# Performance work log

Measured on AMD Instinct MI355X. Metric: run time of the kernel, lower is better.

## Reference

```python
import jax, jax.numpy as jnp
import numpy as np

VOCAB, EMB, HID, T, B = 50257, 512, 1024, 512, 64
R, ALPHA = 8, 16
SCALE = ALPHA / R  # LoRA scaling


def _layer_params(key, in_dim, hid):
    ks = jax.random.split(key, 8)
    stdv = 1.0 / np.sqrt(hid)
    u = lambda k, s: jax.random.uniform(k, s, jnp.float32, -stdv, stdv)
    return dict(
        W_ih=u(ks[0], (4 * hid, in_dim)), b_ih=u(ks[1], (4 * hid,)),
        A_ih=jax.random.normal(ks[2], (R, in_dim)) * 0.01,
        B_ih=jax.random.normal(ks[3], (4 * hid, R)) * 0.01,
        W_hh=u(ks[4], (4 * hid, hid)), b_hh=u(ks[5], (4 * hid,)),
        A_hh=jax.random.normal(ks[6], (R, hid)) * 0.01,
        B_hh=jax.random.normal(ks[7], (4 * hid, R)) * 0.01,
    )


def setup_inputs() -> dict:
    key = jax.random.key(0)
    k_emb, kx, kl, k0, k1 = jax.random.split(key, 5)
    emb = jax.random.normal(k_emb, (VOCAB, EMB), jnp.float32)
    emb = emb.at[0].set(0.0)  # padding_idx=0
    x = jax.random.randint(kx, (B, T), 0, VOCAB)
    lengths = jax.random.randint(kl, (B,), 1, T + 1)
    p0 = _layer_params(k0, EMB, HID)
    p1 = _layer_params(k1, HID, HID)
    inp = {"x": x, "lengths": lengths, "emb": emb}
    for name, p in (("0", p0), ("1", p1)):
        for k, v in p.items():
            inp[f"{k}{name}"] = v
    return inp


def _run_layer(seq, W_ih, b_ih, A_ih, B_ih, W_hh, b_hh, A_hh, B_hh):
    # seq: [T, B, D] -> [T, B, H]; LoRA linear: x@W^T + b + (x@A^T)@B^T * scale
    x_proj = (jnp.einsum('tbd,gd->tbg', seq, W_ih) + b_ih
              + jnp.einsum('tbr,gr->tbg', jnp.einsum('tbd,rd->tbr', seq, A_ih), B_ih) * SCALE)

    def step(carry, xp):
        h, c = carry
        gates = (xp + h @ W_hh.T + b_hh + ((h @ A_hh.T) @ B_hh.T) * SCALE)
        i, f, g, o = jnp.split(gates, 4, axis=-1)
        c = jax.nn.sigmoid(f) * c + jax.nn.sigmoid(i) * jnp.tanh(g)
        h = jax.nn.sigmoid(o) * jnp.tanh(c)
        return (h, c), h

    nb = seq.shape[1]
    hid = W_hh.shape[1]
    h0 = jnp.zeros((nb, hid), seq.dtype)
    _, hs = jax.lax.scan(step, (h0, h0), x_proj)
    return hs


def reference(x, lengths, emb,
              W_ih0, b_ih0, A_ih0, B_ih0, W_hh0, b_hh0, A_hh0, B_hh0,
              W_ih1, b_ih1, A_ih1, B_ih1, W_hh1, b_hh1, A_hh1, B_hh1):
    # embedding lookup (dropout in eval mode = identity)
    h_in = emb[x]                       # [B, T, E]
    h_in = jnp.swapaxes(h_in, 0, 1)     # [T, B, E] for scan
    h_in = _run_layer(h_in, W_ih0, b_ih0, A_ih0, B_ih0, W_hh0, b_hh0, A_hh0, B_hh0)
    h_in = _run_layer(h_in, W_ih1, b_ih1, A_ih1, B_ih1, W_hh1, b_hh1, A_hh1, B_hh1)
    idx = jnp.clip(lengths - 1, 0, None)            # [B]
    last_h = h_in[idx, jnp.arange(h_in.shape[1])]   # [B, H]
    return last_h
```

## Files before the change

### kernel.cpp

```cpp
#include <hip/hip_runtime.h>
#include <stdint.h>

typedef _Float16 f16;
typedef _Float16 f16x8 __attribute__((ext_vector_type(8)));
typedef float f32x4 __attribute__((ext_vector_type(4)));

#define NBATCH 64

__device__ __forceinline__ float sigmoidf_(float x) {
    return 1.0f / (1.0f + __expf(-x));
}
__device__ __forceinline__ float tanh_(float x) {
    x = fminf(fmaxf(x, -15.0f), 15.0f);
    float e = __expf(2.0f * x);
    return (e - 1.0f) / (e + 1.0f);
}

__global__ __launch_bounds__(256) void fold_lora(
    const float* __restrict__ W, const float* __restrict__ Bm,
    const float* __restrict__ Am, f16* __restrict__ dst, int K) {
    int cid = blockIdx.x * 256 + threadIdx.x;
    int kc = K >> 3;
    int r = cid / kc;
    int k0 = (cid - r * kc) * 8;
    float bb[8];
#pragma unroll
    for (int j = 0; j < 8; j++) bb[j] = Bm[r * 8 + j];
#pragma unroll
    for (int i = 0; i < 8; i++) {
        float s = 0.0f;
#pragma unroll
        for (int j = 0; j < 8; j++) s += bb[j] * Am[j * K + k0 + i];
        float v = W[(size_t)r * K + k0 + i] + 2.0f * s;
        dst[(size_t)r * K + k0 + i] = (f16)v;
    }
}

__global__ __launch_bounds__(256) void init_misc(
    const float* __restrict__ bih0, const float* __restrict__ bhh0,
    const float* __restrict__ bih1, const float* __restrict__ bhh1,
    float* __restrict__ bsum0, float* __restrict__ bsum1,
    int* __restrict__ flags0, int* __restrict__ flags1,
    float* __restrict__ c0, float* __restrict__ c1) {
    int i = blockIdx.x * 256 + threadIdx.x;
    if (i < 4096) {
        bsum0[i] = bih0[i] + bhh0[i];
        bsum1[i] = bih1[i] + bhh1[i];
    }
    if (i < 256) { flags0[i] = 0; flags1[i] = 0; }
    c0[i] = 0.0f;
    c1[i] = 0.0f;
}

__global__ __launch_bounds__(256) void embed_gather(
    const int* __restrict__ x, const float* __restrict__ emb,
    f16* __restrict__ seqc, int t0) {
    int lt = blockIdx.x;
    int t = t0 + lt;
#pragma unroll
    for (int c = 0; c < 16; c++) {
        int lin = c * 256 + threadIdx.x;
        int b = lin >> 6;
        int e0 = (lin & 63) * 8;
        int tok = x[b * 512 + t];
        const float* src = emb + (size_t)tok * 512 + e0;
        f16x8 v;
#pragma unroll
        for (int i = 0; i < 8; i++) v[i] = (f16)src[i];
        *(f16x8*)&seqc[((size_t)lt * 64 + b) * 512 + e0] = v;
    }
}

__global__ __launch_bounds__(256) void gemm_nt(
    const f16* __restrict__ A, const f16* __restrict__ Bw,
    float* __restrict__ C, int K, int mtmask, int mtshift) {
    __shared__ f16 As[128 * 40];
    __shared__ f16 Bs[128 * 40];
    int bid = blockIdx.x;
    int mt = bid & mtmask, nt = bid >> mtshift;
    int tid = threadIdx.x;
    int w = tid >> 6, lane = tid & 63;
    int lm = lane & 15, lq = lane >> 4;
    int wm = (w >> 1) * 64, wn = (w & 1) * 64;
    f32x4 acc[4][4];
#pragma unroll
    for (int i = 0; i < 4; i++)
#pragma unroll
        for (int j = 0; j < 4; j++) acc[i][j] = f32x4{0.f, 0.f, 0.f, 0.f};
    const f16* Ab = A + (size_t)mt * 128 * K;
    const f16* Bb = Bw + (size_t)nt * 128 * K;
    int nkc = K >> 5;
    for (int kc = 0; kc < nkc; kc++) {
#pragma unroll
        for (int i = 0; i < 2; i++) {
            int cid = tid + i * 256;
            int r = cid >> 2, c8 = (cid & 3) * 8;
            *(f16x8*)&As[r * 40 + c8] = *(const f16x8*)&Ab[(size_t)r * K + kc * 32 + c8];
            *(f16x8*)&Bs[r * 40 + c8] = *(const f16x8*)&Bb[(size_t)r * K + kc * 32 + c8];
        }
        __syncthreads();
        f16x8 af[4], bf[4];
#pragma unroll
        for (int mi = 0; mi < 4; mi++)
            af[mi] = *(const f16x8*)&As[(wm + mi * 16 + lm) * 40 + lq * 8];
#pragma unroll
        for (int ni = 0; ni < 4; ni++)
            bf[ni] = *(const f16x8*)&Bs[(wn + ni * 16 + lm) * 40 + lq * 8];
#pragma unroll
        for (int mi = 0; mi < 4; mi++)
#pragma unroll
            for (int ni = 0; ni < 4; ni++)
                acc[mi][ni] = __builtin_amdgcn_mfma_f32_16x16x32_f16(
                    af[mi], bf[ni], acc[mi][ni], 0, 0, 0);
        __syncthreads();
    }
#pragma unroll
    for (int mi = 0; mi < 4; mi++)
#pragma unroll
        for (int ni = 0; ni < 4; ni++)
#pragma unroll
            for (int r = 0; r < 4; r++) {
                int m = mt * 128 + wm + mi * 16 + lq * 4 + r;
                int n = nt * 128 + wn + ni * 16 + lm;
                int gate = n >> 10, u = n & 1023;
                C[(size_t)m * 4096 + u * 4 + gate] = acc[mi][ni][r];
            }
}


__device__ __forceinline__ void stage_h(f16* hbuf, const uint32_t* hx, int slot,
                                        int bg, int tid) {
    const uint64_t* hp = (const uint64_t*)hx + (size_t)slot * (NBATCH * 256);
#pragma unroll
    for (int i = 0; i < 16; i++) {
        int lin = tid + i * 256;
        int b = lin >> 8, d = lin & 255;
        uint64_t v = __hip_atomic_load(hp + (size_t)(bg * 16 + b) * 256 + d,
                                       __ATOMIC_RELAXED, __HIP_MEMORY_SCOPE_AGENT);
        *(uint64_t*)((char*)hbuf + (size_t)b * 2064 + (size_t)d * 8) = v;
    }
}

__device__ __forceinline__ f32x4 recur_mfma(const f16* hb, const f16x8* wf) {
    f32x4 a0 = f32x4{0.f, 0.f, 0.f, 0.f};
    f32x4 a1 = f32x4{0.f, 0.f, 0.f, 0.f};
    f32x4 a2 = f32x4{0.f, 0.f, 0.f, 0.f};
    f32x4 a3 = f32x4{0.f, 0.f, 0.f, 0.f};
#pragma unroll
    for (int kk = 0; kk < 32; kk += 4) {
        a0 = __builtin_amdgcn_mfma_f32_16x16x32_f16(*(const f16x8*)(hb + (kk + 0) * 32), wf[kk + 0], a0, 0, 0, 0);
        a1 = __builtin_amdgcn_mfma_f32_16x16x32_f16(*(const f16x8*)(hb + (kk + 1) * 32), wf[kk + 1], a1, 0, 0, 0);
        a2 = __builtin_amdgcn_mfma_f32_16x16x32_f16(*(const f16x8*)(hb + (kk + 2) * 32), wf[kk + 2], a2, 0, 0, 0);
        a3 = __builtin_amdgcn_mfma_f32_16x16x32_f16(*(const f16x8*)(hb + (kk + 3) * 32), wf[kk + 3], a3, 0, 0, 0);
    }
    return (a0 + a1) + (a2 + a3);
}

__device__ __forceinline__ void chain_loop(
    const float* __restrict__ xp, const f16* __restrict__ Wh,
    const float* __restrict__ bsum, uint32_t* __restrict__ hexch,
    int* __restrict__ flags, float* __restrict__ cstate,
    int t0, int smask, const int* __restrict__ lengths,
    float* __restrict__ dout, int bid, int nsteps,
    f16* hbuf, float* xch) {
    int tid = threadIdx.x;
    int g = tid >> 6, lane = tid & 63;
    int lm = lane & 15, lq = lane >> 4;
    int bg = bid >> 6, jg = bid & 63;

    f16x8 wfrag[32];
    {
        int grow = g * 1024 + jg * 16 + lm;
        const f16* wp = Wh + (size_t)grow * 1024 + lq * 8;
#pragma unroll
        for (int kk = 0; kk < 32; kk++) wfrag[kk] = *(const f16x8*)(wp + kk * 32);
    }
    int eb = tid >> 4, eu = tid & 15;
    int batch = bg * 16 + eb;
    int hidx = jg * 16 + eu;
    float bias[4];
#pragma unroll
    for (int g2 = 0; g2 < 4; g2++) bias[g2] = bsum[g2 * 1024 + hidx];
    int mylen = (lengths != nullptr) ? lengths[batch] : -1;
    float c = (t0 > 0) ? cstate[(size_t)batch * 1024 + hidx] : 0.0f;
    const int myflag = bg * 64 + jg;

    for (int lt = 0; lt < nsteps; lt++) {
        int t = t0 + lt;
        const f32x4 xpv = *(const f32x4*)(xp + ((size_t)lt * 64 + batch) * 4096 + (hidx << 2));
        f32x4 pre = f32x4{0.f, 0.f, 0.f, 0.f};
        if (t > 0) {
            if (tid < 64) {
                const int* fl = flags + bg * 64;
                for (;;) {
                    int v = __hip_atomic_load(fl + tid, __ATOMIC_RELAXED,
                                              __HIP_MEMORY_SCOPE_AGENT);
                    if (__all(v >= t)) break;
                    __builtin_amdgcn_s_sleep(1);
                }
            }
            __syncthreads();
            stage_h(hbuf, hexch, (t - 1) & smask, bg, tid);
            __syncthreads();
            pre = recur_mfma(&hbuf[lm * 1032 + lq * 8], wfrag);
        }
#pragma unroll
        for (int r = 0; r < 4; r++)
            xch[(g * 16 + lq * 4 + r) * 16 + lm] = pre[r];
        __syncthreads();
        float pg[4];
#pragma unroll
        for (int g2 = 0; g2 < 4; g2++)
            pg[g2] = xch[(g2 * 16 + eb) * 16 + eu] + xpv[g2] + bias[g2];
        float iv = sigmoidf_(pg[0]);
        float fv = sigmoidf_(pg[1]);
        float gv = tanh_(pg[2]);
        float ov = sigmoidf_(pg[3]);
        c = fv * c + iv * gv;
        float h = ov * tanh_(c);
        float hn = __shfl_xor(h, 1);
        if ((tid & 1) == 0) {
            uint16_t lo, hi;
            {
                f16 a = (f16)h, b2 = (f16)hn;
                lo = *(uint16_t*)&a; hi = *(uint16_t*)&b2;
            }
            uint32_t pk = (uint32_t)lo | ((uint32_t)hi << 16);
            __hip_atomic_store(
                hexch + (size_t)(t & smask) * (NBATCH * 512)
                      + (size_t)batch * 512 + (hidx >> 1),
                pk, __ATOMIC_RELAXED, __HIP_MEMORY_SCOPE_AGENT);
        }
        if (dout != nullptr && t == mylen - 1)
            dout[(size_t)batch * 1024 + hidx] = h;
        __syncthreads();
        if (tid == 0)
            __hip_atomic_store(flags + myflag, t + 1, __ATOMIC_RELAXED,
                               __HIP_MEMORY_SCOPE_AGENT);
    }
    cstate[(size_t)batch * 1024 + hidx] = c;
}

__global__ __launch_bounds__(256, 2) void lstm_dual(
    const float* __restrict__ xpA, const f16* __restrict__ WhA,
    const float* __restrict__ bsA, uint32_t* __restrict__ hxA,
    int* __restrict__ flagsA, float* __restrict__ cstA, int t0a, int smaskA,
    const float* __restrict__ xpB, const f16* __restrict__ WhB,
    const float* __restrict__ bsB, uint32_t* __restrict__ hxB,
    int* __restrict__ flagsB, float* __restrict__ cstB, int t0b,
    const int* __restrict__ lengths, float* __restrict__ dout, int nsteps) {
    __shared__ f16 hbuf[16 * 1032];
    __shared__ float xch[4 * 16 * 16];
    const int cid = blockIdx.x;
    if (cid < 256) {
        if (t0a < 0) return;
        chain_loop(xpA, WhA, bsA, hxA, flagsA, cstA, t0a, smaskA,
                   nullptr, nullptr, cid, nsteps, hbuf, xch);
    } else {
        if (t0b < 0) return;
        chain_loop(xpB, WhB, bsB, hxB, flagsB, cstB, t0b, 1,
                   lengths, dout, cid - 256, nsteps, hbuf, xch);
    }
}

extern "C" void kernel_launch(void* const* d_in, const int* in_sizes, int n_in,
                              void* d_out, int out_size, void* d_ws, size_t ws_size,
                              hipStream_t stream) {
    const int*   x     = (const int*)d_in[0];
    const int*   len   = (const int*)d_in[1];
    const float* emb   = (const float*)d_in[2];
    const float* W_ih0 = (const float*)d_in[3];
    const float* b_ih0 = (const float*)d_in[4];
    const float* A_ih0 = (const float*)d_in[5];
    const float* B_ih0 = (const float*)d_in[6];
    const float* W_hh0 = (const float*)d_in[7];
    const float* b_hh0 = (const float*)d_in[8];
    const float* A_hh0 = (const float*)d_in[9];
    const float* B_hh0 = (const float*)d_in[10];
    const float* W_ih1 = (const float*)d_in[11];
    const float* b_ih1 = (const float*)d_in[12];
    const float* A_ih1 = (const float*)d_in[13];
    const float* B_ih1 = (const float*)d_in[14];
    const float* W_hh1 = (const float*)d_in[15];
    const float* b_hh1 = (const float*)d_in[16];
    const float* A_hh1 = (const float*)d_in[17];
    const float* B_hh1 = (const float*)d_in[18];

    char* ws = (char*)d_ws;
    size_t off = 0;
    auto alloc = [&](size_t bytes) {
        size_t o = off;
        off += (bytes + 255) & ~(size_t)255;
        return o;
    };
    f16*   W0f    = (f16*)(ws + alloc((size_t)4096 * 512 * 2));
    f16*   Wh0f   = (f16*)(ws + alloc((size_t)4096 * 1024 * 2));
    f16*   W1f    = (f16*)(ws + alloc((size_t)4096 * 1024 * 2));
    f16*   Wh1f   = (f16*)(ws + alloc((size_t)4096 * 1024 * 2));
    float* bsum0  = (float*)(ws + alloc(4096 * 4));
    float* bsum1  = (float*)(ws + alloc(4096 * 4));
    int*   flags0 = (int*)(ws + alloc(4096));
    int*   flags1 = (int*)(ws + alloc(4096));
    float* c0st   = (float*)(ws + alloc((size_t)64 * 1024 * 4));
    float* c1st   = (float*)(ws + alloc((size_t)64 * 1024 * 4));
    f16*   hx1    = (f16*)(ws + alloc((size_t)2 * 64 * 1024 * 2));

    int CHv = 64;
    {
        auto al = [](size_t b) { return (b + 255) & ~(size_t)255; };
        size_t need = off
            + al((size_t)64 * 64 * 512 * 2)
            + al((size_t)64 * 64 * 1024 * 2)
            + 2 * al((size_t)64 * 64 * 4096 * 4);
        if (ws_size < need) CHv = 32;
    }
    const int NCHv = 512 / CHv;
    f16*   seqc = (f16*)(ws + alloc((size_t)CHv * 64 * 512 * 2));
    f16*   h0c  = (f16*)(ws + alloc((size_t)CHv * 64 * 1024 * 2));
    float* xp0c = (float*)(ws + alloc((size_t)CHv * 64 * 4096 * 4));
    float* xp1c = (float*)(ws + alloc((size_t)CHv * 64 * 4096 * 4));
    const int mtiles  = (CHv * 64) / 128;
    const int mtmask  = mtiles - 1;
    const int mtshift = (CHv == 64) ? 5 : 4;
    (void)in_sizes; (void)n_in; (void)out_size;

    fold_lora<<<1024, 256, 0, stream>>>(W_ih0, B_ih0, A_ih0, W0f, 512);
    fold_lora<<<2048, 256, 0, stream>>>(W_hh0, B_hh0, A_hh0, Wh0f, 1024);
    fold_lora<<<2048, 256, 0, stream>>>(W_ih1, B_ih1, A_ih1, W1f, 1024);
    fold_lora<<<2048, 256, 0, stream>>>(W_hh1, B_hh1, A_hh1, Wh1f, 1024);
    init_misc<<<256, 256, 0, stream>>>(b_ih0, b_hh0, b_ih1, b_hh1,
                                       bsum0, bsum1, flags0, flags1, c0st, c1st);

    for (int c = 0; c <= NCHv; c++) {
        if (c < NCHv) {
            embed_gather<<<CHv, 256, 0, stream>>>(x, emb, seqc, c * CHv);
            gemm_nt<<<mtiles * 32, 256, 0, stream>>>(seqc, W0f, xp0c, 512,
                                                     mtmask, mtshift);
        }
        if (c > 0)
            gemm_nt<<<mtiles * 32, 256, 0, stream>>>(h0c, W1f, xp1c, 1024,
                                                     mtmask, mtshift);
        lstm_dual<<<512, 256, 0, stream>>>(
            xp0c, Wh0f, bsum0, (uint32_t*)h0c, flags0, c0st,
            (c < NCHv) ? c * CHv : -1, CHv - 1,
            xp1c, Wh1f, bsum1, (uint32_t*)hx1, flags1, c1st,
            (c > 0) ? (c - 1) * CHv : -1,
            len, (float*)d_out, CHv);
    }
}
```

Before: 6.009 ms.

## Overlap input-projection GEMMs with LSTM recurrence inside the persistent kernel

Adds 256 extra blocks to the lstm_dual launch. These blocks compute the next chunk's layer-0 input projection and the current chunk's layer-1 input projection while the recurrent chains run. Layer-1 tiles spin on the layer-0 step flags and read the hidden states with atomic loads, so they can start before the chunk finishes. The xp and seqc buffers are now double-buffered to make this possible. The change costs extra workspace, needs three blocks resident per CU, and adds spin-wait contention beside the latency-critical recurrent chains.

```diff
diff --git a/kernel.cpp b/kernel.cpp
--- a/kernel.cpp
+++ b/kernel.cpp
@@ -71,13 +71,11 @@
     }
 }
 
-__global__ __launch_bounds__(256) void gemm_nt(
-    const f16* __restrict__ A, const f16* __restrict__ Bw,
-    float* __restrict__ C, int K, int mtmask, int mtshift) {
-    __shared__ f16 As[128 * 40];
-    __shared__ f16 Bs[128 * 40];
-    int bid = blockIdx.x;
-    int mt = bid & mtmask, nt = bid >> mtshift;
+template <bool ATOMIC_A>
+__device__ __forceinline__ void gemm_tile(
+    f16* As, f16* Bs, const f16* Aplain, const uint64_t* A64,
+    const f16* __restrict__ Bw, float* __restrict__ C,
+    int K, int mt, int nt) {
     int tid = threadIdx.x;
     int w = tid >> 6, lane = tid & 63;
     int lm = lane & 15, lq = lane >> 4;
@@ -87,7 +85,8 @@
     for (int i = 0; i < 4; i++)
 #pragma unroll
         for (int j = 0; j < 4; j++) acc[i][j] = f32x4{0.f, 0.f, 0.f, 0.f};
-    const f16* Ab = A + (size_t)mt * 128 * K;
+    const f16* Ab = Aplain + (size_t)mt * 128 * K;
+    const uint64_t* Ab64 = A64 + (size_t)mt * 128 * (K >> 2);
     const f16* Bb = Bw + (size_t)nt * 128 * K;
     int nkc = K >> 5;
     for (int kc = 0; kc < nkc; kc++) {
@@ -95,8 +94,20 @@
         for (int i = 0; i < 2; i++) {
             int cid = tid + i * 256;
             int r = cid >> 2, c8 = (cid & 3) * 8;
-            *(f16x8*)&As[r * 40 + c8] = *(const f16x8*)&Ab[(size_t)r * K + kc * 32 + c8];
-            *(f16x8*)&Bs[r * 40 + c8] = *(const f16x8*)&Bb[(size_t)r * K + kc * 32 + c8];
+            if (ATOMIC_A) {
+                size_t o = (size_t)r * (K >> 2) + (size_t)kc * 8 + (c8 >> 2);
+                uint64_t v0 = __hip_atomic_load(Ab64 + o, __ATOMIC_RELAXED,
+                                                __HIP_MEMORY_SCOPE_AGENT);
+                uint64_t v1 = __hip_atomic_load(Ab64 + o + 1, __ATOMIC_RELAXED,
+                                                __HIP_MEMORY_SCOPE_AGENT);
+                *(uint64_t*)&As[r * 40 + c8] = v0;
+                *(uint64_t*)&As[r * 40 + c8 + 4] = v1;
+            } else {
+                *(f16x8*)&As[r * 40 + c8] =
+                    *(const f16x8*)&Ab[(size_t)r * K + kc * 32 + c8];
+            }
+            *(f16x8*)&Bs[r * 40 + c8] =
+                *(const f16x8*)&Bb[(size_t)r * K + kc * 32 + c8];
         }
         __syncthreads();
         f16x8 af[4], bf[4];
@@ -125,6 +136,15 @@
                 int gate = n >> 10, u = n & 1023;
                 C[(size_t)m * 4096 + u * 4 + gate] = acc[mi][ni][r];
             }
+}
+
+__global__ __launch_bounds__(256) void gemm_nt(
+    const f16* __restrict__ A, const f16* __restrict__ Bw,
+    float* __restrict__ C, int K, int mtmask, int mtshift) {
+    __shared__ __align__(16) char smem[20480];
+    int bid = blockIdx.x;
+    gemm_tile<false>((f16*)smem, (f16*)(smem + 10240), A, nullptr, Bw, C, K,
+                     bid & mtmask, bid >> mtshift);
 }
 
 
@@ -241,25 +261,66 @@
     cstate[(size_t)batch * 1024 + hidx] = c;
 }
 
-__global__ __launch_bounds__(256, 2) void lstm_dual(
+__global__ __launch_bounds__(256, 3) void lstm_dual(
     const float* __restrict__ xpA, const f16* __restrict__ WhA,
     const float* __restrict__ bsA, uint32_t* __restrict__ hxA,
     int* __restrict__ flagsA, float* __restrict__ cstA, int t0a, int smaskA,
     const float* __restrict__ xpB, const f16* __restrict__ WhB,
     const float* __restrict__ bsB, uint32_t* __restrict__ hxB,
     int* __restrict__ flagsB, float* __restrict__ cstB, int t0b,
-    const int* __restrict__ lengths, float* __restrict__ dout, int nsteps) {
-    __shared__ f16 hbuf[16 * 1032];
-    __shared__ float xch[4 * 16 * 16];
+    const int* __restrict__ lengths, float* __restrict__ dout, int nsteps,
+    const f16* __restrict__ seqcN, const f16* __restrict__ W0f,
+    const f16* __restrict__ W1f, float* __restrict__ xp0out,
+    float* __restrict__ xp1out, int tpb, int mtmaskG, int mtshiftG) {
+    __shared__ __align__(16) char smem[37376];
     const int cid = blockIdx.x;
     if (cid < 256) {
         if (t0a < 0) return;
         chain_loop(xpA, WhA, bsA, hxA, flagsA, cstA, t0a, smaskA,
-                   nullptr, nullptr, cid, nsteps, hbuf, xch);
-    } else {
+                   nullptr, nullptr, cid, nsteps,
+                   (f16*)smem, (float*)(smem + 33024));
+    } else if (cid < 512) {
         if (t0b < 0) return;
         chain_loop(xpB, WhB, bsB, hxB, flagsB, cstB, t0b, 1,
-                   lengths, dout, cid - 256, nsteps, hbuf, xch);
+                   lengths, dout, cid - 256, nsteps,
+                   (f16*)smem, (float*)(smem + 33024));
+    } else {
+        f16* As = (f16*)smem;
+        f16* Bs = (f16*)(smem + 10240);
+        const int gb = cid - 512;
+        if (seqcN != nullptr) {
+            for (int j = 0; j < tpb; j++) {
+                int id = gb * tpb + j;
+                gemm_tile<false>(As, Bs, seqcN, nullptr, W0f, xp0out, 512,
+                                 id & mtmaskG, id >> mtshiftG);
+            }
+        }
+        if (t0a >= 0) {
+            for (int j = 0; j < tpb; j++) {
+                int id = gb * tpb + j;
+                int mt = id & mtmaskG, nt = id >> mtshiftG;
+                int tneed = t0a + 2 * mt + 2;
+                if (threadIdx.x < 64) {
+                    int tx = threadIdx.x;
+                    for (;;) {
+                        int v0 = __hip_atomic_load(flagsA + tx, __ATOMIC_RELAXED,
+                                                   __HIP_MEMORY_SCOPE_AGENT);
+                        int v1 = __hip_atomic_load(flagsA + 64 + tx, __ATOMIC_RELAXED,
+                                                   __HIP_MEMORY_SCOPE_AGENT);
+                        int v2 = __hip_atomic_load(flagsA + 128 + tx, __ATOMIC_RELAXED,
+                                                   __HIP_MEMORY_SCOPE_AGENT);
+                        int v3 = __hip_atomic_load(flagsA + 192 + tx, __ATOMIC_RELAXED,
+                                                   __HIP_MEMORY_SCOPE_AGENT);
+                        int mn = min(min(v0, v1), min(v2, v3));
+                        if (__all(mn >= tneed)) break;
+                        __builtin_amdgcn_s_sleep(2);
+                    }
+                }
+                __syncthreads();
+                gemm_tile<true>(As, Bs, nullptr, (const uint64_t*)hxA, W1f,
+                                xp1out, 1024, mt, nt);
+            }
+        }
     }
 }
 
@@ -305,23 +366,26 @@
     float* c1st   = (float*)(ws + alloc((size_t)64 * 1024 * 4));
     f16*   hx1    = (f16*)(ws + alloc((size_t)2 * 64 * 1024 * 2));
 
-    int CHv = 64;
-    {
-        auto al = [](size_t b) { return (b + 255) & ~(size_t)255; };
-        size_t need = off
-            + al((size_t)64 * 64 * 512 * 2)
-            + al((size_t)64 * 64 * 1024 * 2)
-            + 2 * al((size_t)64 * 64 * 4096 * 4);
-        if (ws_size < need) CHv = 32;
-    }
+    auto al = [](size_t b) { return (b + 255) & ~(size_t)255; };
+    auto need_for = [&](size_t CH) {
+        return off + 2 * al(CH * 64 * 512 * 2)
+                   + al(CH * 64 * 1024 * 2)
+                   + 4 * al(CH * 64 * 4096 * 4);
+    };
+    int CHv = (ws_size >= need_for(64)) ? 64 : 32;
     const int NCHv = 512 / CHv;
-    f16*   seqc = (f16*)(ws + alloc((size_t)CHv * 64 * 512 * 2));
+    const size_t seqcE = (size_t)CHv * 64 * 512;
+    const size_t xpE   = (size_t)CHv * 64 * 4096;
+    f16*   seqc = (f16*)(ws + alloc(2 * al(seqcE * 2)) );
     f16*   h0c  = (f16*)(ws + alloc((size_t)CHv * 64 * 1024 * 2));
-    float* xp0c = (float*)(ws + alloc((size_t)CHv * 64 * 4096 * 4));
-    float* xp1c = (float*)(ws + alloc((size_t)CHv * 64 * 4096 * 4));
+    float* xp0  = (float*)(ws + alloc(2 * al(xpE * 4)));
+    float* xp1  = (float*)(ws + alloc(2 * al(xpE * 4)));
+    const size_t seqcStride = al(seqcE * 2) / sizeof(f16);
+    const size_t xpStride   = al(xpE * 4) / sizeof(float);
     const int mtiles  = (CHv * 64) / 128;
     const int mtmask  = mtiles - 1;
     const int mtshift = (CHv == 64) ? 5 : 4;
+    const int tpb     = (mtiles * 32) / 256;
     (void)in_sizes; (void)n_in; (void)out_size;
 
     fold_lora<<<1024, 256, 0, stream>>>(W_ih0, B_ih0, A_ih0, W0f, 512);
@@ -331,20 +395,23 @@
     init_misc<<<256, 256, 0, stream>>>(b_ih0, b_hh0, b_ih1, b_hh1,
                                        bsum0, bsum1, flags0, flags1, c0st, c1st);
 
+    embed_gather<<<CHv, 256, 0, stream>>>(x, emb, seqc, 0);
+    gemm_nt<<<mtiles * 32, 256, 0, stream>>>(seqc, W0f, xp0, 512,
+                                             mtmask, mtshift);
     for (int c = 0; c <= NCHv; c++) {
-        if (c < NCHv) {
-            embed_gather<<<CHv, 256, 0, stream>>>(x, emb, seqc, c * CHv);
-            gemm_nt<<<mtiles * 32, 256, 0, stream>>>(seqc, W0f, xp0c, 512,
-                                                     mtmask, mtshift);
-        }
-        if (c > 0)
-            gemm_nt<<<mtiles * 32, 256, 0, stream>>>(h0c, W1f, xp1c, 1024,
-                                                     mtmask, mtshift);
-        lstm_dual<<<512, 256, 0, stream>>>(
-            xp0c, Wh0f, bsum0, (uint32_t*)h0c, flags0, c0st,
-            (c < NCHv) ? c * CHv : -1, CHv - 1,
-            xp1c, Wh1f, bsum1, (uint32_t*)hx1, flags1, c1st,
-            (c > 0) ? (c - 1) * CHv : -1,
-            len, (float*)d_out, CHv);
-    }
-}
+        if (c + 1 < NCHv)
+            embed_gather<<<CHv, 256, 0, stream>>>(
+                x, emb, seqc + ((c + 1) & 1) * seqcStride, (c + 1) * CHv);
+        const bool g0 = (c + 1) < NCHv;
+        lstm_dual<<<768, 256, 0, stream>>>(
+            xp0 + (c & 1) * xpStride, Wh0f, bsum0, (uint32_t*)h0c,
+            flags0, c0st, (c < NCHv) ? c * CHv : -1, CHv - 1,
+            xp1 + ((c + 1) & 1) * xpStride, Wh1f, bsum1, (uint32_t*)hx1,
+            flags1, c1st, (c > 0) ? (c - 1) * CHv : -1,
+            len, (float*)d_out, CHv,
+            g0 ? (seqc + ((c + 1) & 1) * seqcStride) : nullptr, W0f, W1f,
+            xp0 + ((c + 1) & 1) * xpStride,
+            xp1 + (c & 1) * xpStride,
+            tpb, mtmask, mtshift);
+    }
+}
```

Result: slower. 8.340 ms (+38.8%).

## Replace flag barrier with tagged h exchange and merge chunk GEMMs into one launch

Applied to the files above, without the earlier changes.

The recurrent exchange now stores each packed h pair with the timestep in its upper 32 bits. Consumers spin on the tags of the exact words they need, so the per-block flag polling and one __syncthreads are gone. The two input-projection GEMMs and the next chunk's embedding gather are fused into one launch, with the gather double-buffered into alternate seqc buffers. The cost is twice the bytes in the h exchange and for the layer-1 GEMM A operand, plus per-word spin loops that may add memory traffic.

```diff
diff --git a/kernel.cpp b/kernel.cpp
--- a/kernel.cpp
+++ b/kernel.cpp
@@ -40,16 +40,19 @@
     const float* __restrict__ bih0, const float* __restrict__ bhh0,
     const float* __restrict__ bih1, const float* __restrict__ bhh1,
     float* __restrict__ bsum0, float* __restrict__ bsum1,
-    int* __restrict__ flags0, int* __restrict__ flags1,
     float* __restrict__ c0, float* __restrict__ c1) {
     int i = blockIdx.x * 256 + threadIdx.x;
     if (i < 4096) {
         bsum0[i] = bih0[i] + bhh0[i];
         bsum1[i] = bih1[i] + bhh1[i];
     }
-    if (i < 256) { flags0[i] = 0; flags1[i] = 0; }
     c0[i] = 0.0f;
     c1[i] = 0.0f;
+}
+
+__global__ __launch_bounds__(256) void init_tags(uint64_t* __restrict__ p, int n) {
+    int i = blockIdx.x * 256 + threadIdx.x;
+    if (i < n) p[i] = 0xFFFFFFFF00000000ULL;
 }
 
 __global__ __launch_bounds__(256) void embed_gather(
@@ -71,13 +74,11 @@
     }
 }
 
-__global__ __launch_bounds__(256) void gemm_nt(
-    const f16* __restrict__ A, const f16* __restrict__ Bw,
-    float* __restrict__ C, int K, int mtmask, int mtshift) {
-    __shared__ f16 As[128 * 40];
-    __shared__ f16 Bs[128 * 40];
-    int bid = blockIdx.x;
-    int mt = bid & mtmask, nt = bid >> mtshift;
+template <int AMODE>
+__device__ __forceinline__ void gemm_tile(
+    f16* As, f16* Bs, const f16* Aplain, const uint64_t* A64,
+    const f16* __restrict__ Bw, float* __restrict__ C,
+    int K, int mt, int nt) {
     int tid = threadIdx.x;
     int w = tid >> 6, lane = tid & 63;
     int lm = lane & 15, lq = lane >> 4;
@@ -87,7 +88,8 @@
     for (int i = 0; i < 4; i++)
 #pragma unroll
         for (int j = 0; j < 4; j++) acc[i][j] = f32x4{0.f, 0.f, 0.f, 0.f};
-    const f16* Ab = A + (size_t)mt * 128 * K;
+    const f16* Ab = Aplain + (size_t)mt * 128 * K;
+    const uint64_t* Ab64 = A64 + (size_t)mt * 128 * (K >> 1);
     const f16* Bb = Bw + (size_t)nt * 128 * K;
     int nkc = K >> 5;
     for (int kc = 0; kc < nkc; kc++) {
@@ -95,8 +97,19 @@
         for (int i = 0; i < 2; i++) {
             int cid = tid + i * 256;
             int r = cid >> 2, c8 = (cid & 3) * 8;
-            *(f16x8*)&As[r * 40 + c8] = *(const f16x8*)&Ab[(size_t)r * K + kc * 32 + c8];
-            *(f16x8*)&Bs[r * 40 + c8] = *(const f16x8*)&Bb[(size_t)r * K + kc * 32 + c8];
+            if (AMODE == 1) {
+                size_t o = (size_t)r * (K >> 1) + (size_t)kc * 16 + (c8 >> 1);
+                uint64_t q0 = Ab64[o],     q1 = Ab64[o + 1];
+                uint64_t q2 = Ab64[o + 2], q3 = Ab64[o + 3];
+                uint32_t* dst = (uint32_t*)&As[r * 40 + c8];
+                dst[0] = (uint32_t)q0; dst[1] = (uint32_t)q1;
+                dst[2] = (uint32_t)q2; dst[3] = (uint32_t)q3;
+            } else {
+                *(f16x8*)&As[r * 40 + c8] =
+                    *(const f16x8*)&Ab[(size_t)r * K + kc * 32 + c8];
+            }
+            *(f16x8*)&Bs[r * 40 + c8] =
+                *(const f16x8*)&Bb[(size_t)r * K + kc * 32 + c8];
         }
         __syncthreads();
         f16x8 af[4], bf[4];
@@ -127,19 +140,44 @@
             }
 }
 
-
-__device__ __forceinline__ void stage_h(f16* hbuf, const uint32_t* hx, int slot,
-                                        int bg, int tid) {
-    const uint64_t* hp = (const uint64_t*)hx + (size_t)slot * (NBATCH * 256);
-#pragma unroll
-    for (int i = 0; i < 16; i++) {
-        int lin = tid + i * 256;
-        int b = lin >> 8, d = lin & 255;
-        uint64_t v = __hip_atomic_load(hp + (size_t)(bg * 16 + b) * 256 + d,
-                                       __ATOMIC_RELAXED, __HIP_MEMORY_SCOPE_AGENT);
-        *(uint64_t*)((char*)hbuf + (size_t)b * 2064 + (size_t)d * 8) = v;
-    }
-}
+__global__ __launch_bounds__(256) void gemm_combo(
+    const f16* __restrict__ A0, const f16* __restrict__ W0f,
+    float* __restrict__ xp0,
+    const uint64_t* __restrict__ A1, const f16* __restrict__ W1f,
+    float* __restrict__ xp1,
+    const int* __restrict__ x, const float* __restrict__ emb,
+    f16* __restrict__ seqcN, int t0N,
+    int G, int mtmask, int mtshift) {
+    __shared__ __align__(16) char smem[20480];
+    int bid = blockIdx.x;
+    if (bid < G) {
+        if (A0 == nullptr) return;
+        gemm_tile<0>((f16*)smem, (f16*)(smem + 10240), A0, nullptr, W0f, xp0,
+                     512, bid & mtmask, bid >> mtshift);
+    } else if (bid < 2 * G) {
+        if (A1 == nullptr) return;
+        int id = bid - G;
+        gemm_tile<1>((f16*)smem, (f16*)(smem + 10240), nullptr, A1, W1f, xp1,
+                     1024, id & mtmask, id >> mtshift);
+    } else {
+        if (seqcN == nullptr) return;
+        int lt = bid - 2 * G;
+        int t = t0N + lt;
+#pragma unroll
+        for (int c = 0; c < 16; c++) {
+            int lin = c * 256 + threadIdx.x;
+            int b = lin >> 6;
+            int e0 = (lin & 63) * 8;
+            int tok = x[b * 512 + t];
+            const float* src = emb + (size_t)tok * 512 + e0;
+            f16x8 v;
+#pragma unroll
+            for (int i = 0; i < 8; i++) v[i] = (f16)src[i];
+            *(f16x8*)&seqcN[((size_t)lt * 64 + b) * 512 + e0] = v;
+        }
+    }
+}
+
 
 __device__ __forceinline__ f32x4 recur_mfma(const f16* hb, const f16x8* wf) {
     f32x4 a0 = f32x4{0.f, 0.f, 0.f, 0.f};
@@ -158,11 +196,10 @@
 
 __device__ __forceinline__ void chain_loop(
     const float* __restrict__ xp, const f16* __restrict__ Wh,
-    const float* __restrict__ bsum, uint32_t* __restrict__ hexch,
-    int* __restrict__ flags, float* __restrict__ cstate,
-    int t0, int smask, const int* __restrict__ lengths,
-    float* __restrict__ dout, int bid, int nsteps,
-    f16* hbuf, float* xch) {
+    const float* __restrict__ bsum, uint64_t* __restrict__ hexch,
+    float* __restrict__ cstate, int t0, int smask,
+    const int* __restrict__ lengths, float* __restrict__ dout,
+    int bid, int nsteps, f16* hbuf, float* xch) {
     int tid = threadIdx.x;
     int g = tid >> 6, lane = tid & 63;
     int lm = lane & 15, lq = lane >> 4;
@@ -183,24 +220,44 @@
     for (int g2 = 0; g2 < 4; g2++) bias[g2] = bsum[g2 * 1024 + hidx];
     int mylen = (lengths != nullptr) ? lengths[batch] : -1;
     float c = (t0 > 0) ? cstate[(size_t)batch * 1024 + hidx] : 0.0f;
-    const int myflag = bg * 64 + jg;
 
     for (int lt = 0; lt < nsteps; lt++) {
         int t = t0 + lt;
         const f32x4 xpv = *(const f32x4*)(xp + ((size_t)lt * 64 + batch) * 4096 + (hidx << 2));
         f32x4 pre = f32x4{0.f, 0.f, 0.f, 0.f};
         if (t > 0) {
-            if (tid < 64) {
-                const int* fl = flags + bg * 64;
-                for (;;) {
-                    int v = __hip_atomic_load(fl + tid, __ATOMIC_RELAXED,
-                                              __HIP_MEMORY_SCOPE_AGENT);
-                    if (__all(v >= t)) break;
-                    __builtin_amdgcn_s_sleep(1);
+            const uint64_t* hp = hexch
+                + (size_t)((t - 1) & smask) * (NBATCH * 512)
+                + (size_t)bg * 16 * 512;
+            const uint32_t etag = (uint32_t)(t - 1);
+#pragma unroll
+            for (int half = 0; half < 2; half++) {
+                uint64_t v[16];
+#pragma unroll
+                for (int i = 0; i < 16; i++) {
+                    int lin = tid + (half * 16 + i) * 256;
+                    v[i] = __hip_atomic_load(
+                        hp + (size_t)(lin >> 9) * 512 + (lin & 511),
+                        __ATOMIC_RELAXED, __HIP_MEMORY_SCOPE_AGENT);
+                }
+#pragma unroll
+                for (int i = 0; i < 16; i++) {
+                    int lin = tid + (half * 16 + i) * 256;
+                    while ((uint32_t)(v[i] >> 32) != etag) {
+                        __builtin_amdgcn_s_sleep(1);
+                        v[i] = __hip_atomic_load(
+                            hp + (size_t)(lin >> 9) * 512 + (lin & 511),
+                            __ATOMIC_RELAXED, __HIP_MEMORY_SCOPE_AGENT);
+                    }
+                }
+#pragma unroll
+                for (int i = 0; i < 16; i++) {
+                    int lin = tid + (half * 16 + i) * 256;
+                    int b = lin >> 9, d = lin & 511;
+                    *(uint32_t*)((char*)hbuf + (size_t)b * 2064 + (size_t)d * 4)
+                        = (uint32_t)v[i];
                 }
             }
-            __syncthreads();
-            stage_h(hbuf, hexch, (t - 1) & smask, bg, tid);
             __syncthreads();
             pre = recur_mfma(&hbuf[lm * 1032 + lq * 8], wfrag);
         }
@@ -226,39 +283,37 @@
                 lo = *(uint16_t*)&a; hi = *(uint16_t*)&b2;
             }
             uint32_t pk = (uint32_t)lo | ((uint32_t)hi << 16);
+            uint64_t q = ((uint64_t)(uint32_t)t << 32) | (uint64_t)pk;
             __hip_atomic_store(
                 hexch + (size_t)(t & smask) * (NBATCH * 512)
                       + (size_t)batch * 512 + (hidx >> 1),
-                pk, __ATOMIC_RELAXED, __HIP_MEMORY_SCOPE_AGENT);
+                q, __ATOMIC_RELAXED, __HIP_MEMORY_SCOPE_AGENT);
         }
         if (dout != nullptr && t == mylen - 1)
             dout[(size_t)batch * 1024 + hidx] = h;
         __syncthreads();
-        if (tid == 0)
-            __hip_atomic_store(flags + myflag, t + 1, __ATOMIC_RELAXED,
-                               __HIP_MEMORY_SCOPE_AGENT);
     }
     cstate[(size_t)batch * 1024 + hidx] = c;
 }
 
 __global__ __launch_bounds__(256, 2) void lstm_dual(
     const float* __restrict__ xpA, const f16* __restrict__ WhA,
-    const float* __restrict__ bsA, uint32_t* __restrict__ hxA,
-    int* __restrict__ flagsA, float* __restrict__ cstA, int t0a, int smaskA,
+    const float* __restrict__ bsA, uint64_t* __restrict__ hxA,
+    float* __restrict__ cstA, int t0a, int smaskA,
     const float* __restrict__ xpB, const f16* __restrict__ WhB,
-    const float* __restrict__ bsB, uint32_t* __restrict__ hxB,
-    int* __restrict__ flagsB, float* __restrict__ cstB, int t0b,
+    const float* __restrict__ bsB, uint64_t* __restrict__ hxB,
+    float* __restrict__ cstB, int t0b,
     const int* __restrict__ lengths, float* __restrict__ dout, int nsteps) {
     __shared__ f16 hbuf[16 * 1032];
     __shared__ float xch[4 * 16 * 16];
     const int cid = blockIdx.x;
     if (cid < 256) {
         if (t0a < 0) return;
-        chain_loop(xpA, WhA, bsA, hxA, flagsA, cstA, t0a, smaskA,
+        chain_loop(xpA, WhA, bsA, hxA, cstA, t0a, smaskA,
                    nullptr, nullptr, cid, nsteps, hbuf, xch);
     } else {
         if (t0b < 0) return;
-        chain_loop(xpB, WhB, bsB, hxB, flagsB, cstB, t0b, 1,
+        chain_loop(xpB, WhB, bsB, hxB, cstB, t0b, 1,
                    lengths, dout, cid - 256, nsteps, hbuf, xch);
     }
 }
@@ -299,29 +354,28 @@
     f16*   Wh1f   = (f16*)(ws + alloc((size_t)4096 * 1024 * 2));
     float* bsum0  = (float*)(ws + alloc(4096 * 4));
     float* bsum1  = (float*)(ws + alloc(4096 * 4));
-    int*   flags0 = (int*)(ws + alloc(4096));
-    int*   flags1 = (int*)(ws + alloc(4096));
     float* c0st   = (float*)(ws + alloc((size_t)64 * 1024 * 4));
     float* c1st   = (float*)(ws + alloc((size_t)64 * 1024 * 4));
-    f16*   hx1    = (f16*)(ws + alloc((size_t)2 * 64 * 1024 * 2));
-
-    int CHv = 64;
-    {
-        auto al = [](size_t b) { return (b + 255) & ~(size_t)255; };
-        size_t need = off
-            + al((size_t)64 * 64 * 512 * 2)
-            + al((size_t)64 * 64 * 1024 * 2)
-            + 2 * al((size_t)64 * 64 * 4096 * 4);
-        if (ws_size < need) CHv = 32;
-    }
+    uint64_t* hx1 = (uint64_t*)(ws + alloc((size_t)2 * 64 * 512 * 8));
+
+    auto al = [](size_t b) { return (b + 255) & ~(size_t)255; };
+    auto need_for = [&](size_t CH) {
+        return off + 2 * al(CH * 64 * 512 * 2)
+                   + al(CH * 64 * 512 * 8)
+                   + 2 * al(CH * 64 * 4096 * 4);
+    };
+    int CHv = (ws_size >= need_for(64)) ? 64 : 32;
     const int NCHv = 512 / CHv;
-    f16*   seqc = (f16*)(ws + alloc((size_t)CHv * 64 * 512 * 2));
-    f16*   h0c  = (f16*)(ws + alloc((size_t)CHv * 64 * 1024 * 2));
-    float* xp0c = (float*)(ws + alloc((size_t)CHv * 64 * 4096 * 4));
-    float* xp1c = (float*)(ws + alloc((size_t)CHv * 64 * 4096 * 4));
+    const size_t seqcE = (size_t)CHv * 64 * 512;
+    f16*      seqc = (f16*)(ws + alloc(2 * al(seqcE * 2)));
+    uint64_t* h0c  = (uint64_t*)(ws + alloc((size_t)CHv * 64 * 512 * 8));
+    float*    xp0  = (float*)(ws + alloc((size_t)CHv * 64 * 4096 * 4));
+    float*    xp1  = (float*)(ws + alloc((size_t)CHv * 64 * 4096 * 4));
+    const size_t seqcStride = al(seqcE * 2) / sizeof(f16);
     const int mtiles  = (CHv * 64) / 128;
     const int mtmask  = mtiles - 1;
     const int mtshift = (CHv == 64) ? 5 : 4;
+    const int G       = mtiles * 32;
     (void)in_sizes; (void)n_in; (void)out_size;
 
     fold_lora<<<1024, 256, 0, stream>>>(W_ih0, B_ih0, A_ih0, W0f, 512);
@@ -329,21 +383,26 @@
     fold_lora<<<2048, 256, 0, stream>>>(W_ih1, B_ih1, A_ih1, W1f, 1024);
     fold_lora<<<2048, 256, 0, stream>>>(W_hh1, B_hh1, A_hh1, Wh1f, 1024);
     init_misc<<<256, 256, 0, stream>>>(b_ih0, b_hh0, b_ih1, b_hh1,
-                                       bsum0, bsum1, flags0, flags1, c0st, c1st);
-
+                                       bsum0, bsum1, c0st, c1st);
+    {
+        int n0 = CHv * 64 * 512;
+        init_tags<<<(n0 + 255) / 256, 256, 0, stream>>>(h0c, n0);
+        init_tags<<<(2 * 64 * 512 + 255) / 256, 256, 0, stream>>>(hx1,
+                                                                  2 * 64 * 512);
+    }
+
+    embed_gather<<<CHv, 256, 0, stream>>>(x, emb, seqc, 0);
     for (int c = 0; c <= NCHv; c++) {
-        if (c < NCHv) {
-            embed_gather<<<CHv, 256, 0, stream>>>(x, emb, seqc, c * CHv);
-            gemm_nt<<<mtiles * 32, 256, 0, stream>>>(seqc, W0f, xp0c, 512,
-                                                     mtmask, mtshift);
-        }
-        if (c > 0)
-            gemm_nt<<<mtiles * 32, 256, 0, stream>>>(h0c, W1f, xp1c, 1024,
-                                                     mtmask, mtshift);
+        const f16* A0 = (c < NCHv) ? seqc + (c & 1) * seqcStride : nullptr;
+        const uint64_t* A1 = (c > 0) ? h0c : nullptr;
+        f16* sN = (c + 1 < NCHv) ? seqc + ((c + 1) & 1) * seqcStride : nullptr;
+        gemm_combo<<<2 * G + CHv, 256, 0, stream>>>(
+            A0, W0f, xp0, A1, W1f, xp1, x, emb, sN, (c + 1) * CHv,
+            G, mtmask, mtshift);
         lstm_dual<<<512, 256, 0, stream>>>(
-            xp0c, Wh0f, bsum0, (uint32_t*)h0c, flags0, c0st,
+            xp0, Wh0f, bsum0, h0c, c0st,
             (c < NCHv) ? c * CHv : -1, CHv - 1,
-            xp1c, Wh1f, bsum1, (uint32_t*)hx1, flags1, c1st,
+            xp1, Wh1f, bsum1, hx1, c1st,
             (c > 0) ? (c - 1) * CHv : -1,
             len, (float*)d_out, CHv);
     }
```

Result: slower. 7.053 ms (+17.4%).
